# Kernel optimization log

Hardware: AMD Instinct MI355X
Metric: run time of the kernel (lower is better)

The kernel has to match this reference:

```python
import jax, jax.numpy as jnp
import numpy as np

B, T, U, D, V = 8, 128, 64, 512, 1024

def setup_inputs() -> dict:
    key = jax.random.key(0)
    k1, k2, k3, k4, k5, k6 = jax.random.split(key, 6)
    source_encodings = jax.random.normal(k1, (B, T, D), dtype=jnp.float32)
    target_encodings = jax.random.normal(k2, (B, U, D), dtype=jnp.float32)
    source_lengths = jax.random.randint(k3, (B,), 1, T + 1, dtype=jnp.int32)
    target_lengths = jax.random.randint(k4, (B,), 1, U + 1, dtype=jnp.int32)
    # Linear(D, V): weight (V, D), bias (V), init like torch default (uniform)
    bound = 1.0 / np.sqrt(D)
    W = jax.random.uniform(k5, (V, D), minval=-bound, maxval=bound, dtype=jnp.float32)
    b = jax.random.uniform(k6, (V,), minval=-bound, maxval=bound, dtype=jnp.float32)
    return {"source_encodings": source_encodings, "source_lengths": source_lengths,
            "target_encodings": target_encodings, "target_lengths": target_lengths,
            "W": W, "b": b}

def reference(source_encodings, source_lengths, target_encodings, target_lengths, W, b):
    # broadcast add: (B,T,1,D) + (B,1,U,D) -> (B,T,U,D)
    joint = source_encodings[:, :, None, :] + target_encodings[:, None, :, :]
    relu_out = jax.nn.relu(joint)
    # linear projection: (B,T,U,D) x (D,V) + b -> (B,T,U,V)
    output = jnp.einsum('btud,vd->btuv', relu_out, W) + b
    return (output, source_lengths, target_lengths)
```

## Files before the change

### kernel.cpp

```cpp
#include <hip/hip_runtime.h>

typedef unsigned int  u32;
typedef unsigned short u16;
typedef float  f32x4  __attribute__((ext_vector_type(4)));
typedef int    i32x4  __attribute__((ext_vector_type(4)));
typedef __bf16 bf16x8 __attribute__((ext_vector_type(8)));

#define AS1 __attribute__((address_space(1)))
#define AS3 __attribute__((address_space(3)))

__device__ __forceinline__ void gload_lds16(const void* g, void* l) {
  __builtin_amdgcn_global_load_lds((AS1 void*)g, (AS3 void*)l, 16, 0, 0);
}

constexpr int B_ = 8, T_ = 128, U_ = 64, D_ = 512, V_ = 1024;
constexpr int M_ = B_ * T_ * U_;
constexpr int BK = 64;

__global__ void prep_w(const float* __restrict__ W, u16* __restrict__ Wb) {
  const int tid = blockIdx.x * 256 + threadIdx.x;
  const int v  = tid >> 6;
  const int cs = tid & 63;
  const int g  = cs >> 3, cl = cs & 7;
  const float* sp = W + (size_t)v * D_ + cs * 8;
  float4 w0 = *(const float4*)sp;
  float4 w1 = *(const float4*)(sp + 4);
  union { __bf16 h[8]; i32x4 x; } pk;
  pk.h[0] = (__bf16)w0.x; pk.h[1] = (__bf16)w0.y;
  pk.h[2] = (__bf16)w0.z; pk.h[3] = (__bf16)w0.w;
  pk.h[4] = (__bf16)w1.x; pk.h[5] = (__bf16)w1.y;
  pk.h[6] = (__bf16)w1.z; pk.h[7] = (__bf16)w1.w;
  const int dc = g * 8 + (cl ^ (v & 7));
  *(i32x4*)(Wb + (size_t)v * D_ + dc * 8) = pk.x;
}

__global__ void tail_k(const int* __restrict__ sl, const int* __restrict__ tl,
                       float* __restrict__ tail) {
  const int t = threadIdx.x;
  if (t < 8)       tail[t] = (float)sl[t];
  else if (t < 16) tail[t] = (float)tl[t - 8];
}

template<int USE_WS>
__global__ __launch_bounds__(256, 2) void joiner_gemm(
    const float* __restrict__ src, const float* __restrict__ tgt,
    const u16* __restrict__ Wb, const float* __restrict__ Wf,
    const float* __restrict__ bias, float* __restrict__ out)
{
  __shared__ char As[128 * 128];
  __shared__ char Bs[128 * 128];

  const int tid  = threadIdx.x;
  const int lane = tid & 63;
  const int wid  = tid >> 6;
  const int bn   = blockIdx.x & 7;
  const int bm   = blockIdx.x >> 3;
  const int bt0  = bm * 2;
  const int bb   = bt0 >> 7;
  const int sr0  = tid >> 3;
  const int sc8  = tid & 7;
  const int wm   = (wid >> 1) * 64;
  const int wn   = (wid & 1) * 64;

  f32x4 acc[4][4] = {};

  const float* srcp0 = src + (size_t)bt0 * D_ + sc8 * 8;
  const float* srcp1 = srcp0 + D_;
  const float* tgtp0 = tgt + ((size_t)bb * U_ + sr0) * D_ + sc8 * 8;
  const float* tgtp1 = tgtp0 + (size_t)32 * D_;

  for (int kt = 0; kt < D_ / BK; ++kt) {
    const int k0 = kt * BK;

    if (USE_WS) {
      #pragma unroll
      for (int q = 0; q < 4; ++q) {
        const int i    = wid * 4 + q;
        const int vloc = i * 8 + (lane >> 3);
        const u16* g = Wb + (size_t)(bn * 128 + vloc) * D_ + k0 + (lane & 7) * 8;
        gload_lds16(g, Bs + i * 1024);
      }
    } else {
      #pragma unroll
      for (int j = 0; j < 4; ++j) {
        const int vr = sr0 + 32 * j;
        const float* wp = Wf + (size_t)(bn * 128 + vr) * D_ + k0 + sc8 * 8;
        float4 w0 = *(const float4*)wp;
        float4 w1 = *(const float4*)(wp + 4);
        union { __bf16 h[8]; i32x4 x; } pk;
        pk.h[0] = (__bf16)w0.x; pk.h[1] = (__bf16)w0.y;
        pk.h[2] = (__bf16)w0.z; pk.h[3] = (__bf16)w0.w;
        pk.h[4] = (__bf16)w1.x; pk.h[5] = (__bf16)w1.y;
        pk.h[6] = (__bf16)w1.z; pk.h[7] = (__bf16)w1.w;
        *(i32x4*)(Bs + vr * 128 + ((sc8 ^ (vr & 7)) << 4)) = pk.x;
      }
    }

    float4 s0a = *(const float4*)(srcp0 + k0);
    float4 s0b = *(const float4*)(srcp0 + k0 + 4);
    float4 s1a = *(const float4*)(srcp1 + k0);
    float4 s1b = *(const float4*)(srcp1 + k0 + 4);
    float4 t0a = *(const float4*)(tgtp0 + k0);
    float4 t0b = *(const float4*)(tgtp0 + k0 + 4);
    float4 t1a = *(const float4*)(tgtp1 + k0);
    float4 t1b = *(const float4*)(tgtp1 + k0 + 4);
    #pragma unroll
    for (int i = 0; i < 2; ++i) {
      const float4 sa = i ? s1a : s0a;
      const float4 sb = i ? s1b : s0b;
      #pragma unroll
      for (int j = 0; j < 2; ++j) {
        const float4 ta = j ? t1a : t0a;
        const float4 tb = j ? t1b : t0b;
        const int r = i * 64 + j * 32 + sr0;
        union { __bf16 h[8]; i32x4 x; } pk;
        pk.h[0] = (__bf16)fmaxf(sa.x + ta.x, 0.f);
        pk.h[1] = (__bf16)fmaxf(sa.y + ta.y, 0.f);
        pk.h[2] = (__bf16)fmaxf(sa.z + ta.z, 0.f);
        pk.h[3] = (__bf16)fmaxf(sa.w + ta.w, 0.f);
        pk.h[4] = (__bf16)fmaxf(sb.x + tb.x, 0.f);
        pk.h[5] = (__bf16)fmaxf(sb.y + tb.y, 0.f);
        pk.h[6] = (__bf16)fmaxf(sb.z + tb.z, 0.f);
        pk.h[7] = (__bf16)fmaxf(sb.w + tb.w, 0.f);
        *(i32x4*)(As + r * 128 + ((sc8 ^ (r & 7)) << 4)) = pk.x;
      }
    }
    __syncthreads();

    #pragma unroll
    for (int s = 0; s < 2; ++s) {
      const int kc = s * 4 + (lane >> 4);
      bf16x8 af[4], bg[4];
      #pragma unroll
      for (int mi = 0; mi < 4; ++mi) {
        const int r = wm + mi * 16 + (lane & 15);
        af[mi] = *(const bf16x8*)(As + r * 128 + ((kc ^ (r & 7)) << 4));
      }
      #pragma unroll
      for (int ni = 0; ni < 4; ++ni) {
        const int n = wn + ni * 16 + (lane & 15);
        bg[ni] = *(const bf16x8*)(Bs + n * 128 + ((kc ^ (n & 7)) << 4));
      }
      #pragma unroll
      for (int mi = 0; mi < 4; ++mi)
        #pragma unroll
        for (int ni = 0; ni < 4; ++ni)
          acc[mi][ni] = __builtin_amdgcn_mfma_f32_16x16x32_bf16(
              af[mi], bg[ni], acc[mi][ni], 0, 0, 0);
    }
    __syncthreads();
  }

  const int col = lane & 15;
  const int r4  = (lane >> 4) * 4;
  float bv[4];
  #pragma unroll
  for (int ni = 0; ni < 4; ++ni) bv[ni] = bias[bn * 128 + wn + ni * 16 + col];
  #pragma unroll
  for (int mi = 0; mi < 4; ++mi) {
    const size_t mrow = (size_t)bm * 128 + wm + mi * 16 + r4;
    float* op0 = out + mrow * V_ + bn * 128 + wn + col;
    #pragma unroll
    for (int ni = 0; ni < 4; ++ni) {
      float* op = op0 + ni * 16;
      const f32x4 v = acc[mi][ni];
      op[0 * V_] = v[0] + bv[ni];
      op[1 * V_] = v[1] + bv[ni];
      op[2 * V_] = v[2] + bv[ni];
      op[3 * V_] = v[3] + bv[ni];
    }
  }
}

extern "C" void kernel_launch(void* const* d_in, const int* in_sizes, int n_in,
                              void* d_out, int out_size, void* d_ws, size_t ws_size,
                              hipStream_t stream) {
  const float* src  = (const float*)d_in[0];
  const int*   sl   = (const int*)d_in[1];
  const float* tgt  = (const float*)d_in[2];
  const int*   tl   = (const int*)d_in[3];
  const float* W    = (const float*)d_in[4];
  const float* bias = (const float*)d_in[5];
  float* out  = (float*)d_out;
  float* tail = out + (size_t)M_ * V_;

  tail_k<<<1, 64, 0, stream>>>(sl, tl, tail);

  if (ws_size >= (size_t)V_ * D_ * sizeof(u16)) {
    prep_w<<<(V_ * D_ / 8) / 256, 256, 0, stream>>>(W, (u16*)d_ws);
    joiner_gemm<1><<<(M_ / 128) * (V_ / 128), 256, 0, stream>>>(
        src, tgt, (const u16*)d_ws, nullptr, bias, out);
  } else {
    joiner_gemm<0><<<(M_ / 128) * (V_ / 128), 256, 0, stream>>>(
        src, tgt, nullptr, W, bias, out);
  }
}
```

Before: 107.7 us.

## Double-buffer LDS tiles and prefetch next K-slice during MFMA compute

Splits the A and B shared-memory tiles into two buffers so that global loads for the next K-slice (the src/tgt registers and the W bf16 async copy into LDS) are issued before computing on the current buffer. This leaves one barrier per iteration instead of two and hides global latency behind the MFMAs. The bias load is also hoisted to the top of the kernel. In exchange, LDS use doubles to 64KB per block, which may limit occupancy under launch_bounds(256,2).

```diff
diff --git a/kernel.cpp b/kernel.cpp
--- a/kernel.cpp
+++ b/kernel.cpp
@@ -1,6 +1,5 @@
 #include <hip/hip_runtime.h>
 
-typedef unsigned int  u32;
 typedef unsigned short u16;
 typedef float  f32x4  __attribute__((ext_vector_type(4)));
 typedef int    i32x4  __attribute__((ext_vector_type(4)));
@@ -15,7 +14,6 @@
 
 constexpr int B_ = 8, T_ = 128, U_ = 64, D_ = 512, V_ = 1024;
 constexpr int M_ = B_ * T_ * U_;
-constexpr int BK = 64;
 
 __global__ void prep_w(const float* __restrict__ W, u16* __restrict__ Wb) {
   const int tid = blockIdx.x * 256 + threadIdx.x;
@@ -47,8 +45,8 @@
     const u16* __restrict__ Wb, const float* __restrict__ Wf,
     const float* __restrict__ bias, float* __restrict__ out)
 {
-  __shared__ char As[128 * 128];
-  __shared__ char Bs[128 * 128];
+  __shared__ char As[2][16384];
+  __shared__ char Bs[2][16384];
 
   const int tid  = threadIdx.x;
   const int lane = tid & 63;
@@ -69,49 +67,29 @@
   const float* tgtp0 = tgt + ((size_t)bb * U_ + sr0) * D_ + sc8 * 8;
   const float* tgtp1 = tgtp0 + (size_t)32 * D_;
 
-  for (int kt = 0; kt < D_ / BK; ++kt) {
-    const int k0 = kt * BK;
-
-    if (USE_WS) {
-      #pragma unroll
-      for (int q = 0; q < 4; ++q) {
-        const int i    = wid * 4 + q;
-        const int vloc = i * 8 + (lane >> 3);
-        const u16* g = Wb + (size_t)(bn * 128 + vloc) * D_ + k0 + (lane & 7) * 8;
-        gload_lds16(g, Bs + i * 1024);
-      }
-    } else {
-      #pragma unroll
-      for (int j = 0; j < 4; ++j) {
-        const int vr = sr0 + 32 * j;
-        const float* wp = Wf + (size_t)(bn * 128 + vr) * D_ + k0 + sc8 * 8;
-        float4 w0 = *(const float4*)wp;
-        float4 w1 = *(const float4*)(wp + 4);
-        union { __bf16 h[8]; i32x4 x; } pk;
-        pk.h[0] = (__bf16)w0.x; pk.h[1] = (__bf16)w0.y;
-        pk.h[2] = (__bf16)w0.z; pk.h[3] = (__bf16)w0.w;
-        pk.h[4] = (__bf16)w1.x; pk.h[5] = (__bf16)w1.y;
-        pk.h[6] = (__bf16)w1.z; pk.h[7] = (__bf16)w1.w;
-        *(i32x4*)(Bs + vr * 128 + ((sc8 ^ (vr & 7)) << 4)) = pk.x;
-      }
-    }
-
-    float4 s0a = *(const float4*)(srcp0 + k0);
-    float4 s0b = *(const float4*)(srcp0 + k0 + 4);
-    float4 s1a = *(const float4*)(srcp1 + k0);
-    float4 s1b = *(const float4*)(srcp1 + k0 + 4);
-    float4 t0a = *(const float4*)(tgtp0 + k0);
-    float4 t0b = *(const float4*)(tgtp0 + k0 + 4);
-    float4 t1a = *(const float4*)(tgtp1 + k0);
-    float4 t1b = *(const float4*)(tgtp1 + k0 + 4);
+  float bv[4];
+  #pragma unroll
+  for (int ni = 0; ni < 4; ++ni) bv[ni] = bias[bn * 128 + wn + ni * 16 + (lane & 15)];
+
+  float4 pS0a, pS0b, pS1a, pS1b, pT0a, pT0b, pT1a, pT1b;
+
+  auto loadA = [&](int kt) {
+    const int k0 = kt * 64;
+    pS0a = *(const float4*)(srcp0 + k0); pS0b = *(const float4*)(srcp0 + k0 + 4);
+    pS1a = *(const float4*)(srcp1 + k0); pS1b = *(const float4*)(srcp1 + k0 + 4);
+    pT0a = *(const float4*)(tgtp0 + k0); pT0b = *(const float4*)(tgtp0 + k0 + 4);
+    pT1a = *(const float4*)(tgtp1 + k0); pT1b = *(const float4*)(tgtp1 + k0 + 4);
+  };
+
+  auto expandA = [&](int nb) {
     #pragma unroll
     for (int i = 0; i < 2; ++i) {
-      const float4 sa = i ? s1a : s0a;
-      const float4 sb = i ? s1b : s0b;
+      const float4 sa = i ? pS1a : pS0a;
+      const float4 sb = i ? pS1b : pS0b;
       #pragma unroll
       for (int j = 0; j < 2; ++j) {
-        const float4 ta = j ? t1a : t0a;
-        const float4 tb = j ? t1b : t0b;
+        const float4 ta = j ? pT1a : pT0a;
+        const float4 tb = j ? pT1b : pT0b;
         const int r = i * 64 + j * 32 + sr0;
         union { __bf16 h[8]; i32x4 x; } pk;
         pk.h[0] = (__bf16)fmaxf(sa.x + ta.x, 0.f);
@@ -122,11 +100,38 @@
         pk.h[5] = (__bf16)fmaxf(sb.y + tb.y, 0.f);
         pk.h[6] = (__bf16)fmaxf(sb.z + tb.z, 0.f);
         pk.h[7] = (__bf16)fmaxf(sb.w + tb.w, 0.f);
-        *(i32x4*)(As + r * 128 + ((sc8 ^ (r & 7)) << 4)) = pk.x;
+        *(i32x4*)(As[nb] + r * 128 + ((sc8 ^ (r & 7)) << 4)) = pk.x;
       }
     }
-    __syncthreads();
-
+  };
+
+  auto issueB = [&](int kt, int nb) {
+    #pragma unroll
+    for (int q = 0; q < 4; ++q) {
+      const int i    = wid * 4 + q;
+      const int vloc = i * 8 + (lane >> 3);
+      const u16* g = Wb + (size_t)(bn * 128 + vloc) * D_ + kt * 64 + (lane & 7) * 8;
+      gload_lds16(g, Bs[nb] + i * 1024);
+    }
+  };
+
+  auto stageBf32 = [&](int kt, int nb) {
+    #pragma unroll
+    for (int j = 0; j < 4; ++j) {
+      const int vr = sr0 + 32 * j;
+      const float* wp = Wf + (size_t)(bn * 128 + vr) * D_ + kt * 64 + sc8 * 8;
+      float4 w0 = *(const float4*)wp;
+      float4 w1 = *(const float4*)(wp + 4);
+      union { __bf16 h[8]; i32x4 x; } pk;
+      pk.h[0] = (__bf16)w0.x; pk.h[1] = (__bf16)w0.y;
+      pk.h[2] = (__bf16)w0.z; pk.h[3] = (__bf16)w0.w;
+      pk.h[4] = (__bf16)w1.x; pk.h[5] = (__bf16)w1.y;
+      pk.h[6] = (__bf16)w1.z; pk.h[7] = (__bf16)w1.w;
+      *(i32x4*)(Bs[nb] + vr * 128 + ((sc8 ^ (vr & 7)) << 4)) = pk.x;
+    }
+  };
+
+  auto compute = [&](int cb) {
     #pragma unroll
     for (int s = 0; s < 2; ++s) {
       const int kc = s * 4 + (lane >> 4);
@@ -134,12 +139,12 @@
       #pragma unroll
       for (int mi = 0; mi < 4; ++mi) {
         const int r = wm + mi * 16 + (lane & 15);
-        af[mi] = *(const bf16x8*)(As + r * 128 + ((kc ^ (r & 7)) << 4));
+        af[mi] = *(const bf16x8*)(As[cb] + r * 128 + ((kc ^ (r & 7)) << 4));
       }
       #pragma unroll
       for (int ni = 0; ni < 4; ++ni) {
         const int n = wn + ni * 16 + (lane & 15);
-        bg[ni] = *(const bf16x8*)(Bs + n * 128 + ((kc ^ (n & 7)) << 4));
+        bg[ni] = *(const bf16x8*)(Bs[cb] + n * 128 + ((kc ^ (n & 7)) << 4));
       }
       #pragma unroll
       for (int mi = 0; mi < 4; ++mi)
@@ -148,14 +153,31 @@
           acc[mi][ni] = __builtin_amdgcn_mfma_f32_16x16x32_bf16(
               af[mi], bg[ni], acc[mi][ni], 0, 0, 0);
     }
-    __syncthreads();
+  };
+
+  loadA(0);
+  if (USE_WS) issueB(0, 0); else stageBf32(0, 0);
+  expandA(0);
+  __syncthreads();
+
+  int cur = 0;
+  for (int kt = 0; kt < 8; ++kt) {
+    const int nxt = cur ^ 1;
+    if (kt < 7) {
+      loadA(kt + 1);
+      if (USE_WS) issueB(kt + 1, nxt);
+    }
+    compute(cur);
+    if (kt < 7) {
+      if (!USE_WS) stageBf32(kt + 1, nxt);
+      expandA(nxt);
+      __syncthreads();
+    }
+    cur = nxt;
   }
 
   const int col = lane & 15;
   const int r4  = (lane >> 4) * 4;
-  float bv[4];
-  #pragma unroll
-  for (int ni = 0; ni < 4; ++ni) bv[ni] = bias[bn * 128 + wn + ni * 16 + col];
   #pragma unroll
   for (int mi = 0; mi < 4; ++mi) {
     const size_t mrow = (size_t)bm * 128 + wm + mi * 16 + r4;
```

Result: slower. 125.4 us (+16.4%).

## Materialize bf16 joint activations and double-buffer async LDS loads in GEMM

Applied to the files above, without the earlier changes.

A single prep kernel now converts W to swizzled bf16, computes the relu(src+tgt) joint tensor in bf16 into workspace, and writes the length tail, folding the earlier separate launches into one. The GEMM then streams both A and B tiles with global_load_lds into double-buffered shared memory, overlapping the next tile's loads with the current MFMA work. It also remaps block indices for XCD locality and raises wave priority around the MFMAs. The cost is writing and rereading a 64 MB bf16 activation buffer, which the previous fused on-the-fly construction avoided, plus a larger workspace requirement that falls back to the old path if it is not met.

```diff
diff --git a/kernel.cpp b/kernel.cpp
--- a/kernel.cpp
+++ b/kernel.cpp
@@ -1,6 +1,5 @@
 #include <hip/hip_runtime.h>
 
-typedef unsigned int  u32;
 typedef unsigned short u16;
 typedef float  f32x4  __attribute__((ext_vector_type(4)));
 typedef int    i32x4  __attribute__((ext_vector_type(4)));
@@ -15,23 +14,56 @@
 
 constexpr int B_ = 8, T_ = 128, U_ = 64, D_ = 512, V_ = 1024;
 constexpr int M_ = B_ * T_ * U_;
-constexpr int BK = 64;
-
-__global__ void prep_w(const float* __restrict__ W, u16* __restrict__ Wb) {
-  const int tid = blockIdx.x * 256 + threadIdx.x;
-  const int v  = tid >> 6;
-  const int cs = tid & 63;
-  const int g  = cs >> 3, cl = cs & 7;
-  const float* sp = W + (size_t)v * D_ + cs * 8;
-  float4 w0 = *(const float4*)sp;
-  float4 w1 = *(const float4*)(sp + 4);
-  union { __bf16 h[8]; i32x4 x; } pk;
-  pk.h[0] = (__bf16)w0.x; pk.h[1] = (__bf16)w0.y;
-  pk.h[2] = (__bf16)w0.z; pk.h[3] = (__bf16)w0.w;
-  pk.h[4] = (__bf16)w1.x; pk.h[5] = (__bf16)w1.y;
-  pk.h[6] = (__bf16)w1.z; pk.h[7] = (__bf16)w1.w;
-  const int dc = g * 8 + (cl ^ (v & 7));
-  *(i32x4*)(Wb + (size_t)v * D_ + dc * 8) = pk.x;
+
+__global__ void prep_all(const float* __restrict__ W,
+                         const float* __restrict__ src,
+                         const float* __restrict__ tgt,
+                         const int* __restrict__ sl, const int* __restrict__ tl,
+                         u16* __restrict__ Wb, u16* __restrict__ Aw,
+                         float* __restrict__ tail) {
+  if (blockIdx.x == 0 && threadIdx.x < 16) {
+    const int t = threadIdx.x;
+    tail[t] = (t < 8) ? (float)sl[t] : (float)tl[t - 8];
+  }
+  if (blockIdx.x < 256) {
+    const int tid = blockIdx.x * 256 + threadIdx.x;
+    const int v  = tid >> 6;
+    const int cs = tid & 63;
+    const float* sp = W + (size_t)v * D_ + cs * 8;
+    float4 w0 = *(const float4*)sp;
+    float4 w1 = *(const float4*)(sp + 4);
+    union { __bf16 h[8]; i32x4 x; } pk;
+    pk.h[0] = (__bf16)w0.x; pk.h[1] = (__bf16)w0.y;
+    pk.h[2] = (__bf16)w0.z; pk.h[3] = (__bf16)w0.w;
+    pk.h[4] = (__bf16)w1.x; pk.h[5] = (__bf16)w1.y;
+    pk.h[6] = (__bf16)w1.z; pk.h[7] = (__bf16)w1.w;
+    const int dc = (cs >> 3) * 8 + ((cs & 7) ^ (v & 7));
+    *(i32x4*)(Wb + (size_t)v * D_ + dc * 8) = pk.x;
+  } else {
+    const int tid = (blockIdx.x - 256) * 256 + threadIdx.x;
+    const int m  = tid >> 6;
+    const int cs = tid & 63;
+    const int bt = m >> 6;
+    const int u  = m & 63;
+    const int b  = m >> 13;
+    const float* sp = src + (size_t)bt * D_ + cs * 8;
+    const float* tp = tgt + ((size_t)b * U_ + u) * D_ + cs * 8;
+    float4 s0 = *(const float4*)sp;
+    float4 s1 = *(const float4*)(sp + 4);
+    float4 t0 = *(const float4*)tp;
+    float4 t1 = *(const float4*)(tp + 4);
+    union { __bf16 h[8]; i32x4 x; } pk;
+    pk.h[0] = (__bf16)fmaxf(s0.x + t0.x, 0.f);
+    pk.h[1] = (__bf16)fmaxf(s0.y + t0.y, 0.f);
+    pk.h[2] = (__bf16)fmaxf(s0.z + t0.z, 0.f);
+    pk.h[3] = (__bf16)fmaxf(s0.w + t0.w, 0.f);
+    pk.h[4] = (__bf16)fmaxf(s1.x + t1.x, 0.f);
+    pk.h[5] = (__bf16)fmaxf(s1.y + t1.y, 0.f);
+    pk.h[6] = (__bf16)fmaxf(s1.z + t1.z, 0.f);
+    pk.h[7] = (__bf16)fmaxf(s1.w + t1.w, 0.f);
+    const int dc = (cs >> 3) * 8 + ((cs & 7) ^ (m & 7));
+    *(i32x4*)(Aw + (size_t)m * D_ + dc * 8) = pk.x;
+  }
 }
 
 __global__ void tail_k(const int* __restrict__ sl, const int* __restrict__ tl,
@@ -41,11 +73,107 @@
   else if (t < 16) tail[t] = (float)tl[t - 8];
 }
 
-template<int USE_WS>
-__global__ __launch_bounds__(256, 2) void joiner_gemm(
+__global__ __launch_bounds__(256, 2) void joiner_gemm_ws(
+    const u16* __restrict__ Aw, const u16* __restrict__ Wb,
+    const float* __restrict__ bias, float* __restrict__ out)
+{
+  __shared__ __align__(16) char As[2][16384];
+  __shared__ __align__(16) char Bs[2][16384];
+
+  const int tid  = threadIdx.x;
+  const int lane = tid & 63;
+  const int wid  = tid >> 6;
+  const int wgid = blockIdx.x;
+  const int xcd  = wgid & 7;
+  const int j    = wgid >> 3;
+  const int bm   = xcd * 64 + (j >> 3);
+  const int bn   = j & 7;
+  const int wm   = (wid >> 1) * 64;
+  const int wn   = (wid & 1) * 64;
+
+  f32x4 acc[4][4] = {};
+
+  float bv[4];
+  #pragma unroll
+  for (int ni = 0; ni < 4; ++ni)
+    bv[ni] = bias[bn * 128 + wn + ni * 16 + (lane & 15)];
+
+  auto issueA = [&](int kt, int nb) {
+    #pragma unroll
+    for (int q = 0; q < 4; ++q) {
+      const int i   = wid * 4 + q;
+      const int row = i * 8 + (lane >> 3);
+      const u16* g = Aw + (size_t)(bm * 128 + row) * D_ + kt * 64 + (lane & 7) * 8;
+      gload_lds16(g, As[nb] + i * 1024);
+    }
+  };
+  auto issueB = [&](int kt, int nb) {
+    #pragma unroll
+    for (int q = 0; q < 4; ++q) {
+      const int i   = wid * 4 + q;
+      const int row = i * 8 + (lane >> 3);
+      const u16* g = Wb + (size_t)(bn * 128 + row) * D_ + kt * 64 + (lane & 7) * 8;
+      gload_lds16(g, Bs[nb] + i * 1024);
+    }
+  };
+
+  auto compute = [&](int cb) {
+    #pragma unroll
+    for (int s = 0; s < 2; ++s) {
+      const int kc = s * 4 + (lane >> 4);
+      bf16x8 af[4], bg[4];
+      #pragma unroll
+      for (int mi = 0; mi < 4; ++mi) {
+        const int r = wm + mi * 16 + (lane & 15);
+        af[mi] = *(const bf16x8*)(As[cb] + r * 128 + ((kc ^ (r & 7)) << 4));
+      }
+      #pragma unroll
+      for (int ni = 0; ni < 4; ++ni) {
+        const int n = wn + ni * 16 + (lane & 15);
+        bg[ni] = *(const bf16x8*)(Bs[cb] + n * 128 + ((kc ^ (n & 7)) << 4));
+      }
+      __builtin_amdgcn_s_setprio(1);
+      #pragma unroll
+      for (int mi = 0; mi < 4; ++mi)
+        #pragma unroll
+        for (int ni = 0; ni < 4; ++ni)
+          acc[mi][ni] = __builtin_amdgcn_mfma_f32_16x16x32_bf16(
+              af[mi], bg[ni], acc[mi][ni], 0, 0, 0);
+      __builtin_amdgcn_s_setprio(0);
+    }
+  };
+
+  issueA(0, 0); issueB(0, 0);
+
+  for (int kt = 0; kt < 8; ++kt) {
+    const int cur = kt & 1;
+    __syncthreads();
+    if (kt < 7) { issueA(kt + 1, cur ^ 1); issueB(kt + 1, cur ^ 1); }
+    compute(cur);
+  }
+
+  const int col = lane & 15;
+  const int r4  = (lane >> 4) * 4;
+  #pragma unroll
+  for (int mi = 0; mi < 4; ++mi) {
+    const size_t mrow = (size_t)bm * 128 + wm + mi * 16 + r4;
+    float* op0 = out + mrow * V_ + bn * 128 + wn + col;
+    #pragma unroll
+    for (int ni = 0; ni < 4; ++ni) {
+      float* op = op0 + ni * 16;
+      const f32x4 v = acc[mi][ni];
+      op[0 * V_] = v[0] + bv[ni];
+      op[1 * V_] = v[1] + bv[ni];
+      op[2 * V_] = v[2] + bv[ni];
+      op[3 * V_] = v[3] + bv[ni];
+    }
+  }
+}
+
+__global__ __launch_bounds__(256, 2) void joiner_gemm_f32(
     const float* __restrict__ src, const float* __restrict__ tgt,
-    const u16* __restrict__ Wb, const float* __restrict__ Wf,
-    const float* __restrict__ bias, float* __restrict__ out)
+    const float* __restrict__ Wf, const float* __restrict__ bias,
+    float* __restrict__ out)
 {
   __shared__ char As[128 * 128];
   __shared__ char Bs[128 * 128];
@@ -69,50 +197,34 @@
   const float* tgtp0 = tgt + ((size_t)bb * U_ + sr0) * D_ + sc8 * 8;
   const float* tgtp1 = tgtp0 + (size_t)32 * D_;
 
-  for (int kt = 0; kt < D_ / BK; ++kt) {
-    const int k0 = kt * BK;
-
-    if (USE_WS) {
-      #pragma unroll
-      for (int q = 0; q < 4; ++q) {
-        const int i    = wid * 4 + q;
-        const int vloc = i * 8 + (lane >> 3);
-        const u16* g = Wb + (size_t)(bn * 128 + vloc) * D_ + k0 + (lane & 7) * 8;
-        gload_lds16(g, Bs + i * 1024);
-      }
-    } else {
-      #pragma unroll
-      for (int j = 0; j < 4; ++j) {
-        const int vr = sr0 + 32 * j;
-        const float* wp = Wf + (size_t)(bn * 128 + vr) * D_ + k0 + sc8 * 8;
-        float4 w0 = *(const float4*)wp;
-        float4 w1 = *(const float4*)(wp + 4);
-        union { __bf16 h[8]; i32x4 x; } pk;
-        pk.h[0] = (__bf16)w0.x; pk.h[1] = (__bf16)w0.y;
-        pk.h[2] = (__bf16)w0.z; pk.h[3] = (__bf16)w0.w;
-        pk.h[4] = (__bf16)w1.x; pk.h[5] = (__bf16)w1.y;
-        pk.h[6] = (__bf16)w1.z; pk.h[7] = (__bf16)w1.w;
-        *(i32x4*)(Bs + vr * 128 + ((sc8 ^ (vr & 7)) << 4)) = pk.x;
-      }
-    }
-
-    float4 s0a = *(const float4*)(srcp0 + k0);
-    float4 s0b = *(const float4*)(srcp0 + k0 + 4);
-    float4 s1a = *(const float4*)(srcp1 + k0);
-    float4 s1b = *(const float4*)(srcp1 + k0 + 4);
-    float4 t0a = *(const float4*)(tgtp0 + k0);
-    float4 t0b = *(const float4*)(tgtp0 + k0 + 4);
-    float4 t1a = *(const float4*)(tgtp1 + k0);
-    float4 t1b = *(const float4*)(tgtp1 + k0 + 4);
+  for (int kt = 0; kt < 8; ++kt) {
+    const int k0 = kt * 64;
+    #pragma unroll
+    for (int jj = 0; jj < 4; ++jj) {
+      const int vr = sr0 + 32 * jj;
+      const float* wp = Wf + (size_t)(bn * 128 + vr) * D_ + k0 + sc8 * 8;
+      float4 w0 = *(const float4*)wp;
+      float4 w1 = *(const float4*)(wp + 4);
+      union { __bf16 h[8]; i32x4 x; } pk;
+      pk.h[0] = (__bf16)w0.x; pk.h[1] = (__bf16)w0.y;
+      pk.h[2] = (__bf16)w0.z; pk.h[3] = (__bf16)w0.w;
+      pk.h[4] = (__bf16)w1.x; pk.h[5] = (__bf16)w1.y;
+      pk.h[6] = (__bf16)w1.z; pk.h[7] = (__bf16)w1.w;
+      *(i32x4*)(Bs + vr * 128 + ((sc8 ^ (vr & 7)) << 4)) = pk.x;
+    }
+    float4 s0a = *(const float4*)(srcp0 + k0), s0b = *(const float4*)(srcp0 + k0 + 4);
+    float4 s1a = *(const float4*)(srcp1 + k0), s1b = *(const float4*)(srcp1 + k0 + 4);
+    float4 t0a = *(const float4*)(tgtp0 + k0), t0b = *(const float4*)(tgtp0 + k0 + 4);
+    float4 t1a = *(const float4*)(tgtp1 + k0), t1b = *(const float4*)(tgtp1 + k0 + 4);
     #pragma unroll
     for (int i = 0; i < 2; ++i) {
       const float4 sa = i ? s1a : s0a;
       const float4 sb = i ? s1b : s0b;
       #pragma unroll
-      for (int j = 0; j < 2; ++j) {
-        const float4 ta = j ? t1a : t0a;
-        const float4 tb = j ? t1b : t0b;
-        const int r = i * 64 + j * 32 + sr0;
+      for (int jj = 0; jj < 2; ++jj) {
+        const float4 ta = jj ? t1a : t0a;
+        const float4 tb = jj ? t1b : t0b;
+        const int r = i * 64 + jj * 32 + sr0;
         union { __bf16 h[8]; i32x4 x; } pk;
         pk.h[0] = (__bf16)fmaxf(sa.x + ta.x, 0.f);
         pk.h[1] = (__bf16)fmaxf(sa.y + ta.y, 0.f);
@@ -126,7 +238,6 @@
       }
     }
     __syncthreads();
-
     #pragma unroll
     for (int s = 0; s < 2; ++s) {
       const int kc = s * 4 + (lane >> 4);
@@ -184,14 +295,16 @@
   float* out  = (float*)d_out;
   float* tail = out + (size_t)M_ * V_;
 
-  tail_k<<<1, 64, 0, stream>>>(sl, tl, tail);
-
-  if (ws_size >= (size_t)V_ * D_ * sizeof(u16)) {
-    prep_w<<<(V_ * D_ / 8) / 256, 256, 0, stream>>>(W, (u16*)d_ws);
-    joiner_gemm<1><<<(M_ / 128) * (V_ / 128), 256, 0, stream>>>(
-        src, tgt, (const u16*)d_ws, nullptr, bias, out);
+  const size_t needW = (size_t)V_ * D_ * sizeof(u16);
+  const size_t needA = (size_t)M_ * D_ * sizeof(u16);
+
+  if (ws_size >= needW + needA) {
+    u16* Wb = (u16*)d_ws;
+    u16* Aw = Wb + (size_t)V_ * D_;
+    prep_all<<<256 + M_ * 64 / 256, 256, 0, stream>>>(W, src, tgt, sl, tl, Wb, Aw, tail);
+    joiner_gemm_ws<<<(M_ / 128) * (V_ / 128), 256, 0, stream>>>(Aw, Wb, bias, out);
   } else {
-    joiner_gemm<0><<<(M_ / 128) * (V_ / 128), 256, 0, stream>>>(
-        src, tgt, nullptr, W, bias, out);
-  }
-}
+    tail_k<<<1, 64, 0, stream>>>(sl, tl, tail);
+    joiner_gemm_f32<<<(M_ / 128) * (V_ / 128), 256, 0, stream>>>(src, tgt, W, bias, out);
+  }
+}
```

Measured after the change: 116.1 us. 7.7% more time.
